# Kernel optimization log

Hardware: AMD Instinct MI355X
Metric: run time of the kernel (lower is better)

The kernel has to match this reference:

```python
import jax, jax.numpy as jnp
import numpy as np

METRIC = [1, 1, 1, 1, -1]  # Cl(4,1) signature (+,+,+,+,-)


def _cayley_table():
    """32x32x32 geometric-product table for Cl(4,1); exactly one nonzero per (i,j)."""
    T = np.zeros((32, 32, 32), dtype=np.float32)
    for i in range(32):
        for j in range(32):
            k = i ^ j
            sign = 1.0
            bits = [b for b in range(5) if (i >> b) & 1] + [b for b in range(5) if (j >> b) & 1]
            swaps = 0
            for _ in range(len(bits)):
                for idx in range(len(bits) - 1):
                    if bits[idx] > bits[idx + 1]:
                        bits[idx], bits[idx + 1] = bits[idx + 1], bits[idx]
                        swaps += 1
            if swaps % 2 == 1:
                sign = -sign
            common = i & j
            for b in range(5):
                if (common >> b) & 1:
                    sign *= METRIC[b]
            T[i, j, k] = sign
    return T


def _mnorm(v, eps=1e-8):
    # stabilized L2 normalization over the last (blade) axis
    return v / (jnp.linalg.norm(v, axis=-1, keepdims=True) + eps)


def setup_inputs() -> dict:
    key = jax.random.key(0)
    k1, k2, k3, k4, k5 = jax.random.split(key, 5)
    B, T, D = 128, 512, 64
    x = jax.random.randint(k1, (B, T), 0, 4)
    emb = jax.random.normal(k2, (4, 32), dtype=jnp.float32) * 0.1
    emb = emb.at[:, 0].set(1.0)  # torch init: weight[:,0] = 1
    gin = 32 + D * 32
    gate_w = jax.random.normal(k3, (D, gin), dtype=jnp.float32) / np.sqrt(gin)
    gate_b = jnp.ones((D,), dtype=jnp.float32)  # torch init: bias.fill_(1.0)
    w1 = jax.random.normal(k4, (128, D * 32), dtype=jnp.float32) / np.sqrt(D * 32)
    b1 = jnp.zeros((128,), dtype=jnp.float32)
    ln_g = jnp.ones((128,), dtype=jnp.float32)
    ln_b = jnp.zeros((128,), dtype=jnp.float32)
    w2 = jax.random.normal(k5, (2, 128), dtype=jnp.float32) / np.sqrt(128)
    b2 = jnp.zeros((2,), dtype=jnp.float32)
    gp_table = jnp.asarray(_cayley_table())
    return {"x": x, "emb": emb, "gate_w": gate_w, "gate_b": gate_b,
            "w1": w1, "b1": b1, "ln_g": ln_g, "ln_b": ln_b,
            "w2": w2, "b2": b2, "gp_table": gp_table}


def reference(x, emb, gate_w, gate_b, w1, b1, ln_g, ln_b, w2, b2, gp_table):
    B, T = x.shape
    D = gate_b.shape[0]
    r_in = _mnorm(emb[x])  # [B,T,32]
    h0 = jnp.zeros((B, D, 32), dtype=emb.dtype).at[:, :, 0].set(1.0)

    def step(h, r_t):
        # r_t: [B,32], h: [B,D,32]
        gate_in = jnp.concatenate([h.reshape(B, D * 32), r_t], axis=-1)
        g = jax.nn.sigmoid(gate_in @ gate_w.T + gate_b)[..., None]  # [B,D,1]
        h_next = jnp.einsum('bi,bdj,ijk->bdk', r_t, h, gp_table)   # geometric product
        h = _mnorm((1.0 - g) * h + g * h_next)
        return h, None

    h, _ = jax.lax.scan(step, h0, jnp.swapaxes(r_in, 0, 1))
    z = h.reshape(B, D * 32) @ w1.T + b1
    mu = jnp.mean(z, axis=-1, keepdims=True)
    var = jnp.var(z, axis=-1, keepdims=True)
    z = (z - mu) / jnp.sqrt(var + 1e-5) * ln_g + ln_b  # LayerNorm(128)
    return jax.nn.relu(z) @ w2.T + b2  # [B,2]
```

## Files before the change

kernel.cpp:

```cpp
#include <hip/hip_runtime.h>
#include <hip/hip_fp16.h>

typedef unsigned int u32;
typedef _Float16 h2f __attribute__((ext_vector_type(2)));

#define BB 128
#define TT 512
#define DD 64
#define NBL 32
#define GIN 2080

template <int CTRL>
__device__ __forceinline__ float dpp_mov_f(float x) {
  return __builtin_bit_cast(
      float, __builtin_amdgcn_update_dpp(0, __builtin_bit_cast(int, x), CTRL,
                                         0xF, 0xF, true));
}
template <int CTRL>
__device__ __forceinline__ float dpp_add_f(float x) {
  return x + dpp_mov_f<CTRL>(x);
}
__device__ __forceinline__ float swz_add16(float x) {
  return x + __builtin_bit_cast(float, __builtin_amdgcn_ds_swizzle(
                                           __builtin_bit_cast(int, x), 0x401F));
}
__device__ __forceinline__ float bpermf(int addr, float x) {
  return __builtin_bit_cast(
      float, __builtin_amdgcn_ds_bpermute(addr, __builtin_bit_cast(int, x)));
}
__device__ __forceinline__ float xorf(float a, u32 m) {
  return __builtin_bit_cast(float, __builtin_bit_cast(u32, a) ^ m);
}
__device__ __forceinline__ float uni_f(float v) {
  return __builtin_bit_cast(
      float, __builtin_amdgcn_readfirstlane(__builtin_bit_cast(int, v)));
}
__device__ __forceinline__ int uni_i(int v) {
  return __builtin_amdgcn_readfirstlane(v);
}

__device__ inline int gp_negbit(int i, int j) {
  int sw = 0;
#pragma unroll
  for (int b = 0; b < 5; ++b)
    if ((j >> b) & 1) sw += __popc(i >> (b + 1));
  return (sw ^ ((i & j) >> 4)) & 1;
}

__device__ inline float fdot2f(u32 a, u32 b, float acc) {
#if __has_builtin(__builtin_amdgcn_fdot2)
  return __builtin_amdgcn_fdot2(__builtin_bit_cast(h2f, a),
                                __builtin_bit_cast(h2f, b), acc, false);
#else
  h2f av = __builtin_bit_cast(h2f, a), bv = __builtin_bit_cast(h2f, b);
  return acc + (float)av.x * (float)bv.x + (float)av.y * (float)bv.y;
#endif
}

__device__ inline u32 pkf16(float a, float b) {
  return __builtin_bit_cast(u32, __builtin_amdgcn_cvt_pkrtz(a, b));
}

#define GPQ(Q, E0, E1, E2, E3)                                   \
  do {                                                           \
    float t0 = xorf(RNR[(Q)], sb[(Q)]);                          \
    float t1 = xorf(RNR[(Q) + 8], sb[(Q) + 8]);                  \
    float t2 = xorf(RNR[(Q) + 16], sb[(Q) + 16]);                \
    float t3 = xorf(RNR[(Q) + 24], sb[(Q) + 24]);                \
    b0 = fmaf(t0, (E0), b0);                                     \
    b1 = fmaf(t0, (E1), b1);                                     \
    b2 = fmaf(t0, (E2), b2);                                     \
    b3 = fmaf(t0, (E3), b3);                                     \
    b0 = fmaf(t1, (E1), b0);                                     \
    b1 = fmaf(t1, (E0), b1);                                     \
    b2 = fmaf(t1, (E3), b2);                                     \
    b3 = fmaf(t1, (E2), b3);                                     \
    b0 = fmaf(t2, (E2), b0);                                     \
    b1 = fmaf(-t2, (E3), b1);                                    \
    b2 = fmaf(-t2, (E0), b2);                                    \
    b3 = fmaf(t2, (E1), b3);                                     \
    b0 = fmaf(t3, (E3), b0);                                     \
    b1 = fmaf(-t3, (E2), b1);                                    \
    b2 = fmaf(-t3, (E1), b2);                                    \
    b3 = fmaf(t3, (E0), b3);                                     \
  } while (0)

#define STEP(P, RNR, XI)                                                      \
  do {                                                                        \
    const int pn = (P) ^ 1;                                                   \
       \
    const u32* Hb = &h16t[(P)][s >> 1][(s & 1) << 5];                         \
    float a0 = 0.f, a1 = 0.f, a2 = 0.f, a3 = 0.f;                             \
    _Pragma("unroll") for (int jq = 0; jq < 8; ++jq) {                        \
      uint4 hv = *(const uint4*)(Hb + (jq << 2));                             \
      a0 = fdot2f(gw[0][4 * jq + 0], hv.x, a0);                               \
      a0 = fdot2f(gw[0][4 * jq + 1], hv.y, a0);                               \
      a0 = fdot2f(gw[0][4 * jq + 2], hv.z, a0);                               \
      a0 = fdot2f(gw[0][4 * jq + 3], hv.w, a0);                               \
      a1 = fdot2f(gw[1][4 * jq + 0], hv.x, a1);                               \
      a1 = fdot2f(gw[1][4 * jq + 1], hv.y, a1);                               \
      a1 = fdot2f(gw[1][4 * jq + 2], hv.z, a1);                               \
      a1 = fdot2f(gw[1][4 * jq + 3], hv.w, a1);                               \
      a2 = fdot2f(gw[2][4 * jq + 0], hv.x, a2);                               \
      a2 = fdot2f(gw[2][4 * jq + 1], hv.y, a2);                               \
      a2 = fdot2f(gw[2][4 * jq + 2], hv.z, a2);                               \
      a2 = fdot2f(gw[2][4 * jq + 3], hv.w, a2);                               \
      a3 = fdot2f(gw[3][4 * jq + 0], hv.x, a3);                               \
      a3 = fdot2f(gw[3][4 * jq + 1], hv.y, a3);                               \
      a3 = fdot2f(gw[3][4 * jq + 2], hv.z, a3);                               \
      a3 = fdot2f(gw[3][4 * jq + 3], hv.w, a3);                               \
    }                                                                         \
    a0 = dpp_add_f<0xB1>(a0); a0 = dpp_add_f<0x4E>(a0);                       \
    a0 = dpp_add_f<0x141>(a0); a0 = dpp_add_f<0x140>(a0); a0 = swz_add16(a0); \
    a1 = dpp_add_f<0xB1>(a1); a1 = dpp_add_f<0x4E>(a1);                       \
    a1 = dpp_add_f<0x141>(a1); a1 = dpp_add_f<0x140>(a1); a1 = swz_add16(a1); \
    a2 = dpp_add_f<0xB1>(a2); a2 = dpp_add_f<0x4E>(a2);                       \
    a2 = dpp_add_f<0x141>(a2); a2 = dpp_add_f<0x140>(a2); a2 = swz_add16(a2); \
    a3 = dpp_add_f<0xB1>(a3); a3 = dpp_add_f<0x4E>(a3);                       \
    a3 = dpp_add_f<0x141>(a3); a3 = dpp_add_f<0x140>(a3); a3 = swz_add16(a3); \
    const int jsel = rl & 3;                                                  \
    float zv = (jsel == 0) ? a0 : (jsel == 1) ? a1 : (jsel == 2) ? a2 : a3;   \
    float rcsel = ((XI) == 0)   ? rcv0                                        \
                  : ((XI) == 1) ? rcv1                                        \
                  : ((XI) == 2) ? rcv2                                        \
                                : rcv3;                                       \
    float invsel = ((XI) == 0)   ? iv0                                        \
                   : ((XI) == 1) ? iv1                                        \
                   : ((XI) == 2) ? iv2                                        \
                                 : iv3;                                       \
    float g = 1.f / (1.f + exp2f(-1.44269504f * (zv + rcsel)));               \
                                \
    float b0 = 0.f, b1 = 0.f, b2 = 0.f, b3 = 0.f;                             \
    GPQ(0, u0, u1, u2, u3);                                                   \
    {                                                                         \
      float e0 = dpp_mov_f<0xB1>(u0), e1 = dpp_mov_f<0xB1>(u1);               \
      float e2 = dpp_mov_f<0xB1>(u2), e3 = dpp_mov_f<0xB1>(u3);               \
      GPQ(1, e0, e1, e2, e3);                                                 \
      e0 = dpp_mov_f<0x4E>(u0); e1 = dpp_mov_f<0x4E>(u1);                     \
      e2 = dpp_mov_f<0x4E>(u2); e3 = dpp_mov_f<0x4E>(u3);                     \
      GPQ(2, e0, e1, e2, e3);                                                 \
      e0 = dpp_mov_f<0x1B>(u0); e1 = dpp_mov_f<0x1B>(u1);                     \
      e2 = dpp_mov_f<0x1B>(u2); e3 = dpp_mov_f<0x1B>(u3);                     \
      GPQ(3, e0, e1, e2, e3);                                                 \
    }                                                                         \
    {                                                                         \
      float y0 = dpp_mov_f<0x141>(u0), y1 = dpp_mov_f<0x141>(u1);             \
      float y2 = dpp_mov_f<0x141>(u2), y3 = dpp_mov_f<0x141>(u3);             \
      GPQ(7, y0, y1, y2, y3);                                                 \
      float e0 = dpp_mov_f<0xB1>(y0), e1 = dpp_mov_f<0xB1>(y1);               \
      float e2 = dpp_mov_f<0xB1>(y2), e3 = dpp_mov_f<0xB1>(y3);               \
      GPQ(6, e0, e1, e2, e3);                                                 \
      e0 = dpp_mov_f<0x4E>(y0); e1 = dpp_mov_f<0x4E>(y1);                     \
      e2 = dpp_mov_f<0x4E>(y2); e3 = dpp_mov_f<0x4E>(y3);                     \
      GPQ(5, e0, e1, e2, e3);                                                 \
      e0 = dpp_mov_f<0x1B>(y0); e1 = dpp_mov_f<0x1B>(y1);                     \
      e2 = dpp_mov_f<0x1B>(y2); e3 = dpp_mov_f<0x1B>(y3);                     \
      GPQ(4, e0, e1, e2, e3);                                                 \
    }                                                                         \
         \
    float gi = g * invsel;                                                    \
    float om = 1.f - g;                                                       \
    float nu0 = fmaf(gi, b0, om * u0);                                        \
    float nu1 = fmaf(gi, b1, om * u1);                                        \
    float nu2 = fmaf(gi, b2, om * u2);                                        \
    float nu3 = fmaf(gi, b3, om * u3);                                        \
    float sq = nu0 * nu0 + nu1 * nu1 + nu2 * nu2 + nu3 * nu3;                 \
    sq = dpp_add_f<0xB1>(sq);                                                 \
    sq = dpp_add_f<0x4E>(sq);                                                 \
    sq = dpp_add_f<0x141>(sq);                                                \
    float sc = 1.f / (sqrtf(sq) + 1e-8f);                                     \
    u0 = nu0 * sc; u1 = nu1 * sc; u2 = nu2 * sc; u3 = nu3 * sc;               \
    float v0 = dpp_mov_f<0xB1>(u0);                                           \
    float v1 = dpp_mov_f<0xB1>(u1);                                           \
    float v2 = dpp_mov_f<0xB1>(u2);                                           \
    float v3 = dpp_mov_f<0xB1>(u3);                                           \
    if (!(l & 1)) {                                 \
      h16t[pn][(c) >> 1][d] = pkf16(u0, v0);                                  \
      h16t[pn][(c + 8) >> 1][d] = pkf16(u1, v1);                              \
      h16t[pn][(c + 16) >> 1][d] = pkf16(u2, v2);                             \
      h16t[pn][(c + 24) >> 1][d] = pkf16(u3, v3);                             \
    }                                                                         \
    __syncthreads();                                                          \
  } while (0)

__global__ __launch_bounds__(512)
__attribute__((amdgpu_waves_per_eu(2, 2))) void versor_fused(
    const int* __restrict__ x, const float* __restrict__ emb,
    const float* __restrict__ gate_w, const float* __restrict__ gate_b,
    const float* __restrict__ w1, const float* __restrict__ b1g,
    const float* __restrict__ ln_g, const float* __restrict__ ln_b,
    const float* __restrict__ w2, const float* __restrict__ b2,
    float* __restrict__ out) {
  __shared__ float rn[4][NBL];
  __shared__ float inv_lds[4];
  __shared__ float rc[4][DD];
  __shared__ __align__(16) u32 h16t[2][16][68];
  __shared__ __align__(16) float hs[2048];
  __shared__ float redA[8][2];
  __shared__ float redB[8][2];

  const int b = blockIdx.x;
  const int tid = threadIdx.x;
  const int w = tid >> 6;
  const int l = tid & 63;
  const int rl = l >> 3;
  const int d = (w << 3) + rl;
  const int c = l & 7;
  const int r2g = l >> 5;
  const int s = l & 31;
  const int bp32 = ((l ^ 32) << 2);

  if (tid < 4) {
    float v[NBL];
    float sum = 0.f;
    for (int i = 0; i < NBL; ++i) {
      v[i] = emb[tid * NBL + i];
      sum += v[i] * v[i];
    }
    float sc = 1.f / (sqrtf(sum) + 1e-8f);
    inv_lds[tid] = sc;
    for (int i = 0; i < NBL; ++i) rn[tid][i] = v[i] * sc;
  }
  for (int idx = tid; idx < 16 * 68; idx += 512) {
    int m = idx / 68, dd = idx - m * 68;
    h16t[0][m][dd] = (m == 0 && dd < 64) ? 0x00003C00u : 0u;
  }
  __syncthreads();

  if (tid < 256) {
    int e = tid >> 6, row = tid & 63;
    float sum = 0.f;
    for (int i = 0; i < NBL; ++i) sum += gate_w[row * GIN + 2048 + i] * rn[e][i];
    rc[e][row] = sum;
  }

  u32 gw[4][32];
#pragma unroll
  for (int rr = 0; rr < 4; ++rr) {
    const int row = (w << 3) + (r2g << 2) + rr;
    const float* wp = gate_w + row * GIN;
#pragma unroll
    for (int m = 0; m < 32; ++m) {
      int Dd = 32 * s + m;
      int pair = Dd >> 6, dd = Dd & 63;
      int col = dd * 32 + 2 * pair;
      gw[rr][m] = pkf16(wp[col], wp[col + 1]);
    }
  }
  const float gb = gate_b[d];

  u32 sb[NBL];
#pragma unroll
  for (int i = 0; i < NBL; ++i) sb[i] = gp_negbit(i, i ^ c) ? 0x80000000u : 0u;
  __syncthreads();

  const float rcv0 = rc[0][d] + gb, rcv1 = rc[1][d] + gb;
  const float rcv2 = rc[2][d] + gb, rcv3 = rc[3][d] + gb;
  const float iv0 = inv_lds[0], iv1 = inv_lds[1];
  const float iv2 = inv_lds[2], iv3 = inv_lds[3];

  float u0 = (c == 0) ? 1.f : 0.f, u1 = 0.f, u2 = 0.f, u3 = 0.f;

  const int* xg = x + b * TT;
  int xiA = uni_i(xg[0]);
  int xiB = uni_i(xg[1]);
  float rnA[NBL], rnB[NBL];
#pragma unroll
  for (int i = 0; i < NBL; ++i) rnA[i] = uni_f(emb[xiA * NBL + i]);

  for (int t = 0; t < TT; t += 2) {
#pragma unroll
    for (int i = 0; i < NBL; ++i) rnB[i] = uni_f(emb[xiB * NBL + i]);
    int xiC = uni_i(xg[(t + 2 < TT) ? t + 2 : 0]);
#define RNR rnA
    STEP(0, rnA, xiA);
#undef RNR
#pragma unroll
    for (int i = 0; i < NBL; ++i) rnA[i] = uni_f(emb[xiC * NBL + i]);
    int xiD = uni_i(xg[(t + 3 < TT) ? t + 3 : 0]);
#define RNR rnB
    STEP(1, rnB, xiB);
#undef RNR
    xiA = xiC;
    xiB = xiD;
  }

  {
    float* ho = hs + d * 32 + c;
    ho[0] = u0;
    ho[8] = u1;
    ho[16] = u2;
    ho[24] = u3;
  }
  __syncthreads();

  const int hr = tid >> 2;
  const int seg = tid & 3;
  float acc = 0.f;
  {
    const float4* w4 = (const float4*)(w1 + hr * 2048 + seg * 512);
    const float4* h4 = (const float4*)(hs + seg * 512);
#pragma unroll 8
    for (int k = 0; k < 128; ++k) {
      float4 a = w4[k], hv = h4[k];
      acc = fmaf(a.x, hv.x, acc);
      acc = fmaf(a.y, hv.y, acc);
      acc = fmaf(a.z, hv.z, acc);
      acc = fmaf(a.w, hv.w, acc);
    }
  }
  acc = dpp_add_f<0xB1>(acc);
  acc = dpp_add_f<0x4E>(acc);
  float z = acc + b1g[hr];

  float s1 = z, s2 = z * z;
  s1 = dpp_add_f<0xB1>(s1); s1 = dpp_add_f<0x4E>(s1);
  s1 = dpp_add_f<0x141>(s1); s1 = dpp_add_f<0x140>(s1);
  s1 = swz_add16(s1); s1 += bpermf(bp32, s1);
  s2 = dpp_add_f<0xB1>(s2); s2 = dpp_add_f<0x4E>(s2);
  s2 = dpp_add_f<0x141>(s2); s2 = dpp_add_f<0x140>(s2);
  s2 = swz_add16(s2); s2 += bpermf(bp32, s2);
  if (l == 0) { redA[w][0] = s1; redA[w][1] = s2; }
  __syncthreads();
  float tot1 = 0.f, tot2 = 0.f;
#pragma unroll
  for (int k = 0; k < 8; ++k) { tot1 += redA[k][0]; tot2 += redA[k][1]; }
  float mu = tot1 * (1.f / 512.f);
  float var = tot2 * (1.f / 512.f) - mu * mu;
  z = (z - mu) * rsqrtf(var + 1e-5f) * ln_g[hr] + ln_b[hr];
  z = fmaxf(z, 0.f);

  float c0 = (seg == 0) ? z * w2[hr] : 0.f;
  float c1 = (seg == 0) ? z * w2[128 + hr] : 0.f;
  c0 = dpp_add_f<0xB1>(c0); c0 = dpp_add_f<0x4E>(c0);
  c0 = dpp_add_f<0x141>(c0); c0 = dpp_add_f<0x140>(c0);
  c0 = swz_add16(c0); c0 += bpermf(bp32, c0);
  c1 = dpp_add_f<0xB1>(c1); c1 = dpp_add_f<0x4E>(c1);
  c1 = dpp_add_f<0x141>(c1); c1 = dpp_add_f<0x140>(c1);
  c1 = swz_add16(c1); c1 += bpermf(bp32, c1);
  if (l == 0) { redB[w][0] = c0; redB[w][1] = c1; }
  __syncthreads();
  if (tid == 0) {
    float p0 = 0.f, p1 = 0.f;
#pragma unroll
    for (int k = 0; k < 8; ++k) { p0 += redB[k][0]; p1 += redB[k][1]; }
    out[b * 2 + 0] = p0 + b2[0];
    out[b * 2 + 1] = p1 + b2[1];
  }
}

extern "C" void kernel_launch(void* const* d_in, const int* in_sizes, int n_in,
                              void* d_out, int out_size, void* d_ws,
                              size_t ws_size, hipStream_t stream) {
  (void)in_sizes; (void)n_in; (void)out_size; (void)d_ws; (void)ws_size;
  const int* x = (const int*)d_in[0];
  const float* emb = (const float*)d_in[1];
  const float* gate_w = (const float*)d_in[2];
  const float* gate_b = (const float*)d_in[3];
  const float* w1 = (const float*)d_in[4];
  const float* b1 = (const float*)d_in[5];
  const float* ln_g = (const float*)d_in[6];
  const float* ln_b = (const float*)d_in[7];
  const float* w2 = (const float*)d_in[8];
  const float* b2 = (const float*)d_in[9];
  float* out = (float*)d_out;

  versor_fused<<<dim3(BB), dim3(512), 0, stream>>>(
      x, emb, gate_w, gate_b, w1, b1, ln_g, ln_b, w2, b2, out);
}
```

Measured before the change: 925.9 us.

## Double threads per batch row: 16 lanes per d, two blades per lane

Each block now runs 1024 threads so each of the 64 hidden multivectors is handled by 16 lanes holding two blades each, not 8 lanes holding four. The geometric product is rewritten around a 16-blade pairing with sign masks, and the fp16 state in LDS gets a new layout and gate-weight partitioning. The gate dot products split their work across half-waves and are combined with a bpermute. The goal is to shorten the serial per-timestep critical path, at the cost of more lanes, more cross-lane shuffles and a changed LDS layout.

```diff
diff --git a/kernel.cpp b/kernel.cpp
--- a/kernel.cpp
+++ b/kernel.cpp
@@ -61,38 +61,24 @@
   return __builtin_bit_cast(u32, __builtin_amdgcn_cvt_pkrtz(a, b));
 }
 
-#define GPQ(Q, E0, E1, E2, E3)                                   \
-  do {                                                           \
-    float t0 = xorf(RNR[(Q)], sb[(Q)]);                          \
-    float t1 = xorf(RNR[(Q) + 8], sb[(Q) + 8]);                  \
-    float t2 = xorf(RNR[(Q) + 16], sb[(Q) + 16]);                \
-    float t3 = xorf(RNR[(Q) + 24], sb[(Q) + 24]);                \
-    b0 = fmaf(t0, (E0), b0);                                     \
-    b1 = fmaf(t0, (E1), b1);                                     \
-    b2 = fmaf(t0, (E2), b2);                                     \
-    b3 = fmaf(t0, (E3), b3);                                     \
-    b0 = fmaf(t1, (E1), b0);                                     \
-    b1 = fmaf(t1, (E0), b1);                                     \
-    b2 = fmaf(t1, (E3), b2);                                     \
-    b3 = fmaf(t1, (E2), b3);                                     \
-    b0 = fmaf(t2, (E2), b0);                                     \
-    b1 = fmaf(-t2, (E3), b1);                                    \
-    b2 = fmaf(-t2, (E0), b2);                                    \
-    b3 = fmaf(t2, (E1), b3);                                     \
-    b0 = fmaf(t3, (E3), b0);                                     \
-    b1 = fmaf(-t3, (E2), b1);                                    \
-    b2 = fmaf(-t3, (E1), b2);                                    \
-    b3 = fmaf(t3, (E0), b3);                                     \
+#define GPTERM(M, E0, E1)                                      \
+  do {                                                         \
+    float t0 = xorf(RNR[(M)], sbl[(M)]);                       \
+    float t1 = xorf(xorf(RNR[(M) + 16], sbl[(M)]),             \
+                    ((__builtin_popcount(M) & 1) ? Mo : Me));  \
+    b0 = fmaf(t0, (E0), b0);                                   \
+    b0 = fmaf(t1, (E1), b0);                                   \
+    b1v = fmaf(t0, (E1), b1v);                                 \
+    b1v = fmaf(-t1, (E0), b1v);                                \
   } while (0)
 
 #define STEP(P, RNR, XI)                                                      \
   do {                                                                        \
     const int pn = (P) ^ 1;                                                   \
-       \
-    const u32* Hb = &h16t[(P)][s >> 1][(s & 1) << 5];                         \
+        \
     float a0 = 0.f, a1 = 0.f, a2 = 0.f, a3 = 0.f;                             \
-    _Pragma("unroll") for (int jq = 0; jq < 8; ++jq) {                        \
-      uint4 hv = *(const uint4*)(Hb + (jq << 2));                             \
+    _Pragma("unroll") for (int jq = 0; jq < 4; ++jq) {                        \
+      uint4 hv = *(const uint4*)&h16[(P)][256 * jq + 4 * l];                  \
       a0 = fdot2f(gw[0][4 * jq + 0], hv.x, a0);                               \
       a0 = fdot2f(gw[0][4 * jq + 1], hv.y, a0);                               \
       a0 = fdot2f(gw[0][4 * jq + 2], hv.z, a0);                               \
@@ -110,6 +96,7 @@
       a3 = fdot2f(gw[3][4 * jq + 2], hv.z, a3);                               \
       a3 = fdot2f(gw[3][4 * jq + 3], hv.w, a3);                               \
     }                                                                         \
+                             \
     a0 = dpp_add_f<0xB1>(a0); a0 = dpp_add_f<0x4E>(a0);                       \
     a0 = dpp_add_f<0x141>(a0); a0 = dpp_add_f<0x140>(a0); a0 = swz_add16(a0); \
     a1 = dpp_add_f<0xB1>(a1); a1 = dpp_add_f<0x4E>(a1);                       \
@@ -118,8 +105,9 @@
     a2 = dpp_add_f<0x141>(a2); a2 = dpp_add_f<0x140>(a2); a2 = swz_add16(a2); \
     a3 = dpp_add_f<0xB1>(a3); a3 = dpp_add_f<0x4E>(a3);                       \
     a3 = dpp_add_f<0x141>(a3); a3 = dpp_add_f<0x140>(a3); a3 = swz_add16(a3); \
-    const int jsel = rl & 3;                                                  \
-    float zv = (jsel == 0) ? a0 : (jsel == 1) ? a1 : (jsel == 2) ? a2 : a3;   \
+    float selA = s ? a1 : a0;                                                 \
+    float selB = s ? a3 : a2;                                                 \
+    float zsum = selA + bpermf(bp32, selB);                                   \
     float rcsel = ((XI) == 0)   ? rcv0                                        \
                   : ((XI) == 1) ? rcv1                                        \
                   : ((XI) == 2) ? rcv2                                        \
@@ -128,63 +116,68 @@
                    : ((XI) == 1) ? iv1                                        \
                    : ((XI) == 2) ? iv2                                        \
                                  : iv3;                                       \
-    float g = 1.f / (1.f + exp2f(-1.44269504f * (zv + rcsel)));               \
-                                \
-    float b0 = 0.f, b1 = 0.f, b2 = 0.f, b3 = 0.f;                             \
-    GPQ(0, u0, u1, u2, u3);                                                   \
+    float g = 1.f / (1.f + exp2f(-1.44269504f * (zsum + rcsel)));             \
+                                          \
+    float b0 = 0.f, b1v = 0.f;                                                \
+    GPTERM(0, u0, u1);                                                        \
     {                                                                         \
       float e0 = dpp_mov_f<0xB1>(u0), e1 = dpp_mov_f<0xB1>(u1);               \
-      float e2 = dpp_mov_f<0xB1>(u2), e3 = dpp_mov_f<0xB1>(u3);               \
-      GPQ(1, e0, e1, e2, e3);                                                 \
+      GPTERM(1, e0, e1);                                                      \
       e0 = dpp_mov_f<0x4E>(u0); e1 = dpp_mov_f<0x4E>(u1);                     \
-      e2 = dpp_mov_f<0x4E>(u2); e3 = dpp_mov_f<0x4E>(u3);                     \
-      GPQ(2, e0, e1, e2, e3);                                                 \
+      GPTERM(2, e0, e1);                                                      \
       e0 = dpp_mov_f<0x1B>(u0); e1 = dpp_mov_f<0x1B>(u1);                     \
-      e2 = dpp_mov_f<0x1B>(u2); e3 = dpp_mov_f<0x1B>(u3);                     \
-      GPQ(3, e0, e1, e2, e3);                                                 \
+      GPTERM(3, e0, e1);                                                      \
     }                                                                         \
     {                                                                         \
       float y0 = dpp_mov_f<0x141>(u0), y1 = dpp_mov_f<0x141>(u1);             \
-      float y2 = dpp_mov_f<0x141>(u2), y3 = dpp_mov_f<0x141>(u3);             \
-      GPQ(7, y0, y1, y2, y3);                                                 \
+      GPTERM(7, y0, y1);                                                      \
       float e0 = dpp_mov_f<0xB1>(y0), e1 = dpp_mov_f<0xB1>(y1);               \
-      float e2 = dpp_mov_f<0xB1>(y2), e3 = dpp_mov_f<0xB1>(y3);               \
-      GPQ(6, e0, e1, e2, e3);                                                 \
+      GPTERM(6, e0, e1);                                                      \
       e0 = dpp_mov_f<0x4E>(y0); e1 = dpp_mov_f<0x4E>(y1);                     \
-      e2 = dpp_mov_f<0x4E>(y2); e3 = dpp_mov_f<0x4E>(y3);                     \
-      GPQ(5, e0, e1, e2, e3);                                                 \
+      GPTERM(5, e0, e1);                                                      \
       e0 = dpp_mov_f<0x1B>(y0); e1 = dpp_mov_f<0x1B>(y1);                     \
-      e2 = dpp_mov_f<0x1B>(y2); e3 = dpp_mov_f<0x1B>(y3);                     \
-      GPQ(4, e0, e1, e2, e3);                                                 \
+      GPTERM(4, e0, e1);                                                      \
     }                                                                         \
-         \
+    {                                                                         \
+      float y0 = dpp_mov_f<0x140>(u0), y1 = dpp_mov_f<0x140>(u1);             \
+      GPTERM(15, y0, y1);                                                     \
+      float e0 = dpp_mov_f<0xB1>(y0), e1 = dpp_mov_f<0xB1>(y1);               \
+      GPTERM(14, e0, e1);                                                     \
+      e0 = dpp_mov_f<0x4E>(y0); e1 = dpp_mov_f<0x4E>(y1);                     \
+      GPTERM(13, e0, e1);                                                     \
+      e0 = dpp_mov_f<0x1B>(y0); e1 = dpp_mov_f<0x1B>(y1);                     \
+      GPTERM(12, e0, e1);                                                     \
+      float z0 = dpp_mov_f<0x141>(y0), z1 = dpp_mov_f<0x141>(y1);             \
+      GPTERM(8, z0, z1);                                                      \
+      e0 = dpp_mov_f<0xB1>(z0); e1 = dpp_mov_f<0xB1>(z1);                     \
+      GPTERM(9, e0, e1);                                                      \
+      e0 = dpp_mov_f<0x4E>(z0); e1 = dpp_mov_f<0x4E>(z1);                     \
+      GPTERM(10, e0, e1);                                                     \
+      e0 = dpp_mov_f<0x1B>(z0); e1 = dpp_mov_f<0x1B>(z1);                     \
+      GPTERM(11, e0, e1);                                                     \
+    }                                                                         \
+          \
     float gi = g * invsel;                                                    \
     float om = 1.f - g;                                                       \
     float nu0 = fmaf(gi, b0, om * u0);                                        \
-    float nu1 = fmaf(gi, b1, om * u1);                                        \
-    float nu2 = fmaf(gi, b2, om * u2);                                        \
-    float nu3 = fmaf(gi, b3, om * u3);                                        \
-    float sq = nu0 * nu0 + nu1 * nu1 + nu2 * nu2 + nu3 * nu3;                 \
+    float nu1 = fmaf(gi, b1v, om * u1);                                       \
+    float sq = nu0 * nu0 + nu1 * nu1;                                         \
     sq = dpp_add_f<0xB1>(sq);                                                 \
     sq = dpp_add_f<0x4E>(sq);                                                 \
     sq = dpp_add_f<0x141>(sq);                                                \
+    sq = dpp_add_f<0x140>(sq);                                                \
     float sc = 1.f / (sqrtf(sq) + 1e-8f);                                     \
-    u0 = nu0 * sc; u1 = nu1 * sc; u2 = nu2 * sc; u3 = nu3 * sc;               \
+    u0 = nu0 * sc;                                                            \
+    u1 = nu1 * sc;                                                            \
+          \
     float v0 = dpp_mov_f<0xB1>(u0);                                           \
     float v1 = dpp_mov_f<0xB1>(u1);                                           \
-    float v2 = dpp_mov_f<0xB1>(u2);                                           \
-    float v3 = dpp_mov_f<0xB1>(u3);                                           \
-    if (!(l & 1)) {                                 \
-      h16t[pn][(c) >> 1][d] = pkf16(u0, v0);                                  \
-      h16t[pn][(c + 8) >> 1][d] = pkf16(u1, v1);                              \
-      h16t[pn][(c + 16) >> 1][d] = pkf16(u2, v2);                             \
-      h16t[pn][(c + 24) >> 1][d] = pkf16(u3, v3);                             \
-    }                                                                         \
+    h16[pn][Pst] = (c & 1) ? pkf16(v1, u1) : pkf16(u0, v0);                   \
     __syncthreads();                                                          \
   } while (0)
 
-__global__ __launch_bounds__(512)
-__attribute__((amdgpu_waves_per_eu(2, 2))) void versor_fused(
+__global__ __launch_bounds__(1024, 4)
+__attribute__((amdgpu_waves_per_eu(4, 4))) void versor_fused(
     const int* __restrict__ x, const float* __restrict__ emb,
     const float* __restrict__ gate_w, const float* __restrict__ gate_b,
     const float* __restrict__ w1, const float* __restrict__ b1g,
@@ -194,21 +187,23 @@
   __shared__ float rn[4][NBL];
   __shared__ float inv_lds[4];
   __shared__ float rc[4][DD];
-  __shared__ __align__(16) u32 h16t[2][16][68];
+  __shared__ __align__(16) u32 h16[2][1024];
   __shared__ __align__(16) float hs[2048];
-  __shared__ float redA[8][2];
-  __shared__ float redB[8][2];
+  __shared__ float redA[16][2];
+  __shared__ float redB[16][2];
 
   const int b = blockIdx.x;
   const int tid = threadIdx.x;
   const int w = tid >> 6;
   const int l = tid & 63;
-  const int rl = l >> 3;
-  const int d = (w << 3) + rl;
-  const int c = l & 7;
-  const int r2g = l >> 5;
-  const int s = l & 31;
+  const int rl = l >> 4;
+  const int d = (w << 2) + rl;
+  const int c = l & 15;
+  const int H = l >> 5;
+  const int s = rl & 1;
   const int bp32 = ((l ^ 32) << 2);
+  const int mst = (c >> 1) + ((c & 1) << 3);
+  const int Pst = 256 * ((d & 15) >> 2) + 16 * mst + 4 * (d >> 4) + (d & 3);
 
   if (tid < 4) {
     float v[NBL];
@@ -221,9 +216,10 @@
     inv_lds[tid] = sc;
     for (int i = 0; i < NBL; ++i) rn[tid][i] = v[i] * sc;
   }
-  for (int idx = tid; idx < 16 * 68; idx += 512) {
-    int m = idx / 68, dd = idx - m * 68;
-    h16t[0][m][dd] = (m == 0 && dd < 64) ? 0x00003C00u : 0u;
+  {
+    int m = tid >> 6, dd = tid & 63;
+    int P = 256 * ((dd & 15) >> 2) + 16 * m + 4 * (dd >> 4) + (dd & 3);
+    h16[0][P] = (m == 0) ? 0x00003C00u : 0u;
   }
   __syncthreads();
 
@@ -234,24 +230,30 @@
     rc[e][row] = sum;
   }
 
-  u32 gw[4][32];
-#pragma unroll
-  for (int rr = 0; rr < 4; ++rr) {
-    const int row = (w << 3) + (r2g << 2) + rr;
-    const float* wp = gate_w + row * GIN;
-#pragma unroll
-    for (int m = 0; m < 32; ++m) {
-      int Dd = 32 * s + m;
-      int pair = Dd >> 6, dd = Dd & 63;
-      int col = dd * 32 + 2 * pair;
-      gw[rr][m] = pkf16(wp[col], wp[col + 1]);
+  u32 gw[4][16];
+  {
+    const int mpair = l >> 2;
+    const int dbase = (l & 3) << 4;
+#pragma unroll
+    for (int rr = 0; rr < 4; ++rr) {
+      const int grow = (w << 2) + (rr ^ (H << 1));
+      const float* wp = gate_w + grow * GIN + 2 * mpair;
+#pragma unroll
+      for (int e = 0; e < 16; ++e) {
+        int col = (dbase + e) * 32;
+        gw[rr][e] = pkf16(wp[col], wp[col + 1]);
+      }
     }
   }
   const float gb = gate_b[d];
 
-  u32 sb[NBL];
-#pragma unroll
-  for (int i = 0; i < NBL; ++i) sb[i] = gp_negbit(i, i ^ c) ? 0x80000000u : 0u;
+  u32 sbl[16];
+#pragma unroll
+  for (int m = 0; m < 16; ++m)
+    sbl[m] = gp_negbit(m, m ^ c) ? 0x80000000u : 0u;
+  const int pc = __popc(c) & 1;
+  const u32 Me = ((u32)(pc ^ 1)) << 31;
+  const u32 Mo = ((u32)pc) << 31;
   __syncthreads();
 
   const float rcv0 = rc[0][d] + gb, rcv1 = rc[1][d] + gb;
@@ -259,7 +261,7 @@
   const float iv0 = inv_lds[0], iv1 = inv_lds[1];
   const float iv2 = inv_lds[2], iv3 = inv_lds[3];
 
-  float u0 = (c == 0) ? 1.f : 0.f, u1 = 0.f, u2 = 0.f, u3 = 0.f;
+  float u0 = (c == 0) ? 1.f : 0.f, u1 = 0.f;
 
   const int* xg = x + b * TT;
   int xiA = uni_i(xg[0]);
@@ -285,23 +287,18 @@
     xiB = xiD;
   }
 
-  {
-    float* ho = hs + d * 32 + c;
-    ho[0] = u0;
-    ho[8] = u1;
-    ho[16] = u2;
-    ho[24] = u3;
-  }
-  __syncthreads();
-
-  const int hr = tid >> 2;
-  const int seg = tid & 3;
+  hs[d * 32 + c] = u0;
+  hs[d * 32 + c + 16] = u1;
+  __syncthreads();
+
+  const int hr = tid >> 3;
+  const int seg = tid & 7;
   float acc = 0.f;
   {
-    const float4* w4 = (const float4*)(w1 + hr * 2048 + seg * 512);
-    const float4* h4 = (const float4*)(hs + seg * 512);
+    const float4* w4 = (const float4*)(w1 + hr * 2048 + seg * 256);
+    const float4* h4 = (const float4*)(hs + seg * 256);
 #pragma unroll 8
-    for (int k = 0; k < 128; ++k) {
+    for (int k = 0; k < 64; ++k) {
       float4 a = w4[k], hv = h4[k];
       acc = fmaf(a.x, hv.x, acc);
       acc = fmaf(a.y, hv.y, acc);
@@ -311,6 +308,7 @@
   }
   acc = dpp_add_f<0xB1>(acc);
   acc = dpp_add_f<0x4E>(acc);
+  acc = dpp_add_f<0x141>(acc);
   float z = acc + b1g[hr];
 
   float s1 = z, s2 = z * z;
@@ -324,9 +322,9 @@
   __syncthreads();
   float tot1 = 0.f, tot2 = 0.f;
 #pragma unroll
-  for (int k = 0; k < 8; ++k) { tot1 += redA[k][0]; tot2 += redA[k][1]; }
-  float mu = tot1 * (1.f / 512.f);
-  float var = tot2 * (1.f / 512.f) - mu * mu;
+  for (int k = 0; k < 16; ++k) { tot1 += redA[k][0]; tot2 += redA[k][1]; }
+  float mu = tot1 * (1.f / 1024.f);
+  float var = tot2 * (1.f / 1024.f) - mu * mu;
   z = (z - mu) * rsqrtf(var + 1e-5f) * ln_g[hr] + ln_b[hr];
   z = fmaxf(z, 0.f);
 
@@ -343,7 +341,7 @@
   if (tid == 0) {
     float p0 = 0.f, p1 = 0.f;
 #pragma unroll
-    for (int k = 0; k < 8; ++k) { p0 += redB[k][0]; p1 += redB[k][1]; }
+    for (int k = 0; k < 16; ++k) { p0 += redB[k][0]; p1 += redB[k][1]; }
     out[b * 2 + 0] = p0 + b2[0];
     out[b * 2 + 1] = p1 + b2[1];
   }
@@ -365,6 +363,6 @@
   const float* b2 = (const float*)d_in[9];
   float* out = (float*)d_out;
 
-  versor_fused<<<dim3(BB), dim3(512), 0, stream>>>(
+  versor_fused<<<dim3(BB), dim3(1024), 0, stream>>>(
       x, emb, gate_w, gate_b, w1, b1, ln_g, ln_b, w2, b2, out);
 }
```

Measured after the change: 1.183 ms. 1.28x slower.
